# Performance work log

Hardware: AMD Instinct MI355X
Metric: run time of the kernel (lower is better)

The kernel has to match this reference:

```python
import jax, jax.numpy as jnp
import numpy as np

N, C, K, P, Q, PS = 32, 128, 128, 64, 64, 3

def setup_inputs() -> dict:
    key = jax.random.key(0)
    k1, k2, k3 = jax.random.split(key, 3)
    x = jax.random.normal(k1, (N, C, P, Q), dtype=jnp.float32)
    W = jax.random.normal(k2, (K, C * PS * PS), dtype=jnp.float32) * (1.0 / np.sqrt(C * PS * PS))
    perturbs = jax.random.normal(k3, (N, K, P, Q), dtype=jnp.float32)
    return {"x": x, "W": W, "perturbs": perturbs}

def reference(x, W, perturbs):
    # patchify (pad=1, unfold 3x3, stride 1) + matmul with W^T is exactly a
    # 3x3 SAME convolution: flatten order of patchify is (C, kh, kw), matching
    # conv.weight.reshape(k, -1). Express it as a direct conv (no im2col blowup).
    k = W.shape[0]
    c = x.shape[1]
    w = W.reshape(k, c, PS, PS)  # OIHW
    out = jax.lax.conv_general_dilated(
        x, w,
        window_strides=(1, 1),
        padding=((1, 1), (1, 1)),
        dimension_numbers=("NCHW", "OIHW", "NCHW"),
    )
    return out + perturbs
```

## Files before the change

kernel.cpp:

```cpp
#include <hip/hip_runtime.h>
#include <hip/hip_bf16.h>

#define NN 32
#define CCH 128
#define KK 128
#define PP 64
#define QQ 64

typedef __bf16 bf16x8 __attribute__((ext_vector_type(8)));
typedef float f32x16 __attribute__((ext_vector_type(16)));
typedef float f32x4 __attribute__((ext_vector_type(4)));

#define XT_ELEMS (32ull * 64 * 64 * 128)

__global__ __launch_bounds__(256) void prep_x(const float* __restrict__ x,
                                              __bf16* __restrict__ xT) {
    __shared__ float tile[128 * 64];
    const int t = threadIdx.x;
    const int p = blockIdx.x;
    const int n = blockIdx.y;

#pragma unroll
    for (int pass = 0; pass < 8; ++pass) {
        int idx = pass * 256 + t;
        int qf = idx & 15;
        int c  = idx >> 4;
        f32x4 v = *(const f32x4*)(x + (((size_t)n * CCH + c) * PP + p) * QQ + qf * 4);
        int key = ((c >> 3) & 15) * 4;
        *(f32x4*)(tile + c * 64 + ((qf * 4) ^ key)) = v;
    }
    __syncthreads();

#pragma unroll
    for (int pass = 0; pass < 4; ++pass) {
        int cc   = pass * 2 + (t >> 7);
        int rem  = t & 127;
        int q    = rem >> 1;
        int half = rem & 1;
        int c0   = cc * 16 + half * 8;
        int key  = ((c0 >> 3) & 15) * 4;
        bf16x8 o;
#pragma unroll
        for (int j = 0; j < 8; ++j) o[j] = (__bf16)tile[(c0 + j) * 64 + (q ^ key)];
        *(bf16x8*)(xT + ((((size_t)n * 8 + cc) * PP + p) * QQ + q) * 16 + half * 8) = o;
    }
}

__global__ __launch_bounds__(256) void prep_w(const float* __restrict__ W,
                                              __bf16* __restrict__ Wf) {
    const int id = blockIdx.x * 256 + threadIdx.x;
    const int lane = id & 63;
    const int r1   = id >> 6;
    const int kb   = r1 & 3;
    const int r2   = r1 >> 2;
    const int t    = r2 % 9;
    const int cc   = r2 / 9;

    const int k  = kb * 32 + (lane & 31);
    const int c0 = cc * 16 + (lane >> 5) * 8;

    bf16x8 o;
#pragma unroll
    for (int j = 0; j < 8; ++j)
        o[j] = (__bf16)W[(size_t)k * (CCH * 9) + (size_t)(c0 + j) * 9 + t];
    ((bf16x8*)Wf)[id] = o;
}

#define XPITCH 2112
#define WBYTES 36864
#define XROWS  10
#define XBYTES (XROWS * XPITCH)

__global__ __launch_bounds__(512, 2) void conv_main(const __bf16* __restrict__ xT,
                                                    const __bf16* __restrict__ Wf,
                                                    const float* __restrict__ per,
                                                    float* __restrict__ out) {
    __shared__ __align__(16) char wlds[2][WBYTES];
    __shared__ __align__(16) char xlds[2][XBYTES];

    const int tid  = threadIdx.x;
    const int lane = tid & 63;
    const int w    = tid >> 6;
    const int kbs  = w & 1;
    const int pb   = w >> 1;
    const int n    = blockIdx.y;
    const int p0   = blockIdx.x * 8;
    const int m    = lane & 31;
    const int half = lane >> 5;

    if (tid < 40) {
        int row = tid >> 2, part = tid & 3;
        int off = row * XPITCH + (part >> 1) * 2080 + (part & 1) * 16;
        *(f32x4*)(xlds[0] + off) = f32x4{0.f, 0.f, 0.f, 0.f};
        *(f32x4*)(xlds[1] + off) = f32x4{0.f, 0.f, 0.f, 0.f};
    }

    f32x16 acc[2][2][2];
#pragma unroll
    for (int a = 0; a < 2; ++a)
#pragma unroll
        for (int b = 0; b < 2; ++b)
#pragma unroll
            for (int c = 0; c < 2; ++c)
#pragma unroll
                for (int e = 0; e < 16; ++e) acc[a][b][c][e] = 0.f;

    const char* xb = (const char*)xT + ((size_t)n * 8) * PP * QQ * 32;

    auto stage = [&](int ccn, int buf) {
        const char* g = (const char*)Wf + (size_t)ccn * WBYTES;
#pragma unroll
        for (int it = 0; it < 5; ++it) {
            int idx = it * 512 + tid;
            if (idx < WBYTES / 16) {
                __builtin_amdgcn_global_load_lds(
                    (const __attribute__((address_space(1))) unsigned int*)(g + idx * 16),
                    (__attribute__((address_space(3))) unsigned int*)(wlds[buf] + idx * 16),
                    16, 0, 0);
            }
        }
        const char* gx = xb + (size_t)ccn * (PP * QQ * 32);
#pragma unroll
        for (int it = 0; it < 3; ++it) {
            int gi = it * 512 + tid;
            if (gi < XROWS * 128) {
                int row = gi >> 7;
                int wi  = (gi & 127) * 16;
                int r   = p0 - 1 + row;
                int rc  = r < 0 ? 0 : (r > 63 ? 63 : r);
                __builtin_amdgcn_global_load_lds(
                    (const __attribute__((address_space(1))) unsigned int*)(gx + (size_t)rc * 2048 + wi),
                    (__attribute__((address_space(3))) unsigned int*)(xlds[buf] + row * XPITCH + 32 + wi),
                    16, 0, 0);
            }
        }
    };

    stage(0, 0);
    __syncthreads();

    int cur = 0;
    for (int cc = 0; cc < 8; ++cc) {
        if (cc < 7) stage(cc + 1, cur ^ 1);

        const char* wbase = wlds[cur];
        const char* xbase = xlds[cur];

        bf16x8 a_cur[3][2], a_prev[3][2];
#pragma unroll
        for (int ri = 0; ri < 4; ++ri) {
            const int rr = pb * 2 + ri;
            const int r  = p0 + pb * 2 + ri - 1;
            const bool rok = ((unsigned)r < (unsigned)PP);

            bf16x8 b[3][2];
            if (rok) {
                const char* rbase = xbase + rr * XPITCH + half * 16;
#pragma unroll
                for (int dq = 0; dq < 3; ++dq)
#pragma unroll
                    for (int qb = 0; qb < 2; ++qb)
                        b[dq][qb] = *(const bf16x8*)(rbase + (qb * 32 + m + dq) * 32);
            }

            if (ri < 3) {
#pragma unroll
                for (int dq = 0; dq < 3; ++dq)
#pragma unroll
                    for (int kb = 0; kb < 2; ++kb)
                        a_cur[dq][kb] = ((const bf16x8*)wbase)[((ri * 3 + dq) * 4 +
                                                                kbs * 2 + kb) * 64 + lane];
            }

            if (rok) {
                if (ri >= 1) {
#pragma unroll
                    for (int dq = 0; dq < 3; ++dq)
#pragma unroll
                        for (int kb = 0; kb < 2; ++kb)
#pragma unroll
                            for (int qb = 0; qb < 2; ++qb)
                                acc[1][kb][qb] = __builtin_amdgcn_mfma_f32_32x32x16_bf16(
                                    a_prev[dq][kb], b[dq][qb], acc[1][kb][qb], 0, 0, 0);
                }
                if (ri < 3) {
#pragma unroll
                    for (int dq = 0; dq < 3; ++dq)
#pragma unroll
                        for (int kb = 0; kb < 2; ++kb)
#pragma unroll
                            for (int qb = 0; qb < 2; ++qb)
                                acc[0][kb][qb] = __builtin_amdgcn_mfma_f32_32x32x16_bf16(
                                    a_cur[dq][kb], b[dq][qb], acc[0][kb][qb], 0, 0, 0);
                }
            }

            if (ri < 3) {
#pragma unroll
                for (int dq = 0; dq < 3; ++dq)
#pragma unroll
                    for (int kb = 0; kb < 2; ++kb) a_prev[dq][kb] = a_cur[dq][kb];
            }
        }

        __syncthreads();
        cur ^= 1;
    }

#pragma unroll
    for (int oi = 0; oi < 2; ++oi) {
        const int prow = p0 + pb * 2 + oi;
#pragma unroll
        for (int kbi = 0; kbi < 2; ++kbi) {
#pragma unroll
            for (int qb = 0; qb < 2; ++qb) {
                f32x16 v = acc[oi][kbi][qb];
#pragma unroll
                for (int r = 0; r < 16; ++r) {
                    int krow = (r & 3) + 8 * (r >> 2) + 4 * half;
                    int k    = (kbs * 2 + kbi) * 32 + krow;
                    int q    = qb * 32 + m;
                    size_t oidx = (((size_t)n * KK + k) * PP + prow) * QQ + q;
                    out[oidx] = v[r] + per[oidx];
                }
            }
        }
    }
}

extern "C" void kernel_launch(void* const* d_in, const int* in_sizes, int n_in,
                              void* d_out, int out_size, void* d_ws, size_t ws_size,
                              hipStream_t stream) {
    const float* x   = (const float*)d_in[0];
    const float* W   = (const float*)d_in[1];
    const float* per = (const float*)d_in[2];
    float* out = (float*)d_out;

    __bf16* xT = (__bf16*)d_ws;
    __bf16* Wf = (__bf16*)((char*)d_ws + XT_ELEMS * 2);

    prep_x<<<dim3(PP, NN), 256, 0, stream>>>(x, xT);
    prep_w<<<dim3(72), 256, 0, stream>>>(W, Wf);
    conv_main<<<dim3(PP / 8, NN), 512, 0, stream>>>(xT, Wf, per, out);
}
```

Baseline: 214.4 us.

## Vectorize epilogue via LDS transpose and prefetch perturbs during last compute

Peels the final channel chunk so the perturbs tile is loaded into registers with 16-byte loads before the last MFMA pass, overlapping that global read with compute. The accumulator tiles are then transposed through a per-wave XOR-swizzled LDS scratch region (reusing the now-free weight buffer) so output and perturbs are accessed with coalesced f32x4 loads and stores instead of scalar strided accesses. This adds many live registers for the prefetched perturbs, which may pressure occupancy at two blocks per SM.

```diff
diff --git a/kernel.cpp b/kernel.cpp
--- a/kernel.cpp
+++ b/kernel.cpp
@@ -136,15 +136,9 @@
         }
     };
 
-    stage(0, 0);
-    __syncthreads();
-
-    int cur = 0;
-    for (int cc = 0; cc < 8; ++cc) {
-        if (cc < 7) stage(cc + 1, cur ^ 1);
-
-        const char* wbase = wlds[cur];
-        const char* xbase = xlds[cur];
+    auto compute = [&](int buf) {
+        const char* wbase = wlds[buf];
+        const char* xbase = xlds[buf];
 
         bf16x8 a_cur[3][2], a_prev[3][2];
 #pragma unroll
@@ -202,11 +196,18 @@
                     for (int kb = 0; kb < 2; ++kb) a_prev[dq][kb] = a_cur[dq][kb];
             }
         }
-
+    };
+
+    stage(0, 0);
+    __syncthreads();
+
+    for (int cc = 0; cc < 7; ++cc) {
+        stage(cc + 1, (cc + 1) & 1);
+        compute(cc & 1);
         __syncthreads();
-        cur ^= 1;
-    }
-
+    }
+
+    f32x4 pv[2][2][2][4];
 #pragma unroll
     for (int oi = 0; oi < 2; ++oi) {
         const int prow = p0 + pb * 2 + oi;
@@ -214,14 +215,41 @@
         for (int kbi = 0; kbi < 2; ++kbi) {
 #pragma unroll
             for (int qb = 0; qb < 2; ++qb) {
+#pragma unroll
+                for (int j = 0; j < 4; ++j) {
+                    int k = (kbs * 2 + kbi) * 32 + (lane >> 3) + j * 8;
+                    int q = qb * 32 + (lane & 7) * 4;
+                    pv[oi][kbi][qb][j] =
+                        *(const f32x4*)(per + (((size_t)n * KK + k) * PP + prow) * QQ + q);
+                }
+            }
+        }
+    }
+
+    compute(1);
+
+    float* scr = (float*)(wlds[0] + w * 4096);
+#pragma unroll
+    for (int oi = 0; oi < 2; ++oi) {
+        const int prow = p0 + pb * 2 + oi;
+#pragma unroll
+        for (int kbi = 0; kbi < 2; ++kbi) {
+#pragma unroll
+            for (int qb = 0; qb < 2; ++qb) {
                 f32x16 v = acc[oi][kbi][qb];
 #pragma unroll
                 for (int r = 0; r < 16; ++r) {
-                    int krow = (r & 3) + 8 * (r >> 2) + 4 * half;
-                    int k    = (kbs * 2 + kbi) * 32 + krow;
-                    int q    = qb * 32 + m;
-                    size_t oidx = (((size_t)n * KK + k) * PP + prow) * QQ + q;
-                    out[oidx] = v[r] + per[oidx];
+                    int kl = (r & 3) + 8 * (r >> 2) + 4 * half;
+                    scr[kl * 32 + ((((m >> 2) ^ (kl & 7)) << 2) | (m & 3))] = v[r];
+                }
+#pragma unroll
+                for (int j = 0; j < 4; ++j) {
+                    int kl = (lane >> 3) + j * 8;
+                    f32x4 d = *(const f32x4*)(scr + kl * 32 + (((lane & 7) ^ (kl & 7)) << 2));
+                    f32x4 s = d + pv[oi][kbi][qb][j];
+                    int k = (kbs * 2 + kbi) * 32 + kl;
+                    int q = qb * 32 + (lane & 7) * 4;
+                    *(f32x4*)(out + (((size_t)n * KK + k) * PP + prow) * QQ + q) = s;
                 }
             }
         }
```

Measured after the change: 223.2 us. +4.1%, slower.
